# Kernel optimization log

Measured on AMD Instinct MI355X. Metric: run time of the kernel, lower is better.

Reference implementation:

```python
import jax, jax.numpy as jnp
import numpy as np


def setup_inputs() -> dict:
    key = jax.random.key(0)
    k1, k2 = jax.random.split(key)
    B, P, N, M = 8, 32, 1024, 1024
    normalized_receptive_fields = jax.random.normal(k1, (B, P, N, 3), dtype=jnp.float32)
    reconstructed_points = jax.random.normal(k2, (B, P, M, 3), dtype=jnp.float32)
    return {
        "normalized_receptive_fields": normalized_receptive_fields,
        "reconstructed_points": reconstructed_points,
    }


def reference(normalized_receptive_fields, reconstructed_points):
    B, P, M, _ = reconstructed_points.shape
    N = normalized_receptive_fields.shape[2]
    # Faithful to torch: permute(0,1,3,2) then reshape(-1, M, 3).
    x = jnp.transpose(reconstructed_points, (0, 1, 3, 2)).reshape(-1, M, 3)  # (BP, M, 3)
    y = normalized_receptive_fields.reshape(-1, N, 3)                        # (BP, N, 3)
    xx = jnp.sum(x * x, axis=-1)                 # (BP, M)
    yy = jnp.sum(y * y, axis=-1)                 # (BP, N)
    xy = jnp.einsum('bmc,bnc->bmn', x, y)        # (BP, M, N)
    dist = xx[:, :, None] + yy[:, None, :] - 2.0 * xy  # (BP, M, N)
    min_x_to_y = jnp.min(dist, axis=2)           # (BP, M)
    min_y_to_x = jnp.min(dist, axis=1)           # (BP, N)
    return jnp.mean(min_x_to_y) + jnp.mean(min_y_to_x)
```

## Files before the change

### kernel.cpp

```cpp
#include <hip/hip_runtime.h>
#include <hip/hip_bf16.h>


#define MM 1024
#define NN 1024
#define THREADS 1024
#define NWAVES 16
#define ROWS_PER_WAVE 64
#define RB 4
#define CPL 16
#define FINF 3.4e38f

template <int CTRL>
__device__ __forceinline__ float dpp_ror_min(float v) {
    int vi = __float_as_int(v);
    int t  = __builtin_amdgcn_update_dpp(vi, vi, CTRL, 0xf, 0xf, true);
    return fminf(v, __int_as_float(t));
}

__device__ __forceinline__ float wave_min64(float v, int lane_xor32_addr) {
    v = dpp_ror_min<0x121>(v);
    v = dpp_ror_min<0x122>(v);
    v = dpp_ror_min<0x124>(v);
    v = dpp_ror_min<0x128>(v);
    int s = __builtin_amdgcn_ds_swizzle(__float_as_int(v), 0x401F);
    v = fminf(v, __int_as_float(s));
    int p = __builtin_amdgcn_ds_bpermute(lane_xor32_addr, __float_as_int(v));
    return fminf(v, __int_as_float(p));
}

__global__ __launch_bounds__(THREADS, 4)
void chamfer_kernel(const float* __restrict__ nrf,
                    const float* __restrict__ rp,
                    float* __restrict__ out,
                    float inv_bpm, float inv_bpn) {
    const int bp   = blockIdx.x;
    const int tid  = threadIdx.x;
    const int lane = tid & 63;
    const int wave = tid >> 6;
    const int xaddr32 = ((lane ^ 32) << 2);

    __shared__ float  rpS[MM * 3];
    __shared__ float4 xS[MM];
    __shared__ float4 yS[NN];
    __shared__ float  colminS[NWAVES][NN];
    __shared__ float  rowsumS[NWAVES];
    __shared__ float  csumS[NWAVES];

    const float* rpB = rp  + (size_t)bp * MM * 3;
    const float* yB  = nrf + (size_t)bp * NN * 3;

    for (int i = tid; i < MM * 3; i += THREADS) rpS[i] = rpB[i];
    {
        float a = yB[tid * 3 + 0];
        float b = yB[tid * 3 + 1];
        float c = yB[tid * 3 + 2];
        yS[tid] = make_float4(a, b, c, a * a + b * b + c * c);
    }
    __syncthreads();

    {
        const int k = 3 * tid;
        float a = rpS[((k + 0) & (MM - 1)) * 3 + ((k + 0) >> 10)];
        float b = rpS[((k + 1) & (MM - 1)) * 3 + ((k + 1) >> 10)];
        float c = rpS[((k + 2) & (MM - 1)) * 3 + ((k + 2) >> 10)];
        xS[tid] = make_float4(-2.0f * a, -2.0f * b, -2.0f * c,
                              a * a + b * b + c * c);
    }
    __syncthreads();

    float colmin[CPL];
    #pragma unroll
    for (int i = 0; i < CPL; ++i) colmin[i] = FINF;

    float rowsum = 0.0f;
    const int m0 = wave * ROWS_PER_WAVE;
    for (int r0 = 0; r0 < ROWS_PER_WAVE; r0 += RB) {
        float4 x[RB];
        #pragma unroll
        for (int j = 0; j < RB; ++j) x[j] = xS[m0 + r0 + j];

        float rmin[RB];
        #pragma unroll
        for (int j = 0; j < RB; ++j) rmin[j] = FINF;

        #pragma unroll
        for (int i = 0; i < CPL; ++i) {
            const float4 yv = yS[i * 64 + lane];
            float e[RB];
            #pragma unroll
            for (int j = 0; j < RB; ++j) {
                e[j] = __builtin_fmaf(x[j].x, yv.x,
                        __builtin_fmaf(x[j].y, yv.y,
                         __builtin_fmaf(x[j].z, yv.z, yv.w)));
                rmin[j] = fminf(rmin[j], e[j]);
            }
            float d01 = fminf(e[0] + x[0].w, e[1] + x[1].w);
            float d23 = fminf(e[2] + x[2].w, e[3] + x[3].w);
            colmin[i] = fminf(fminf(colmin[i], d01), d23);
        }

        #pragma unroll
        for (int j = 0; j < RB; ++j) rmin[j] = wave_min64(rmin[j], xaddr32);
        #pragma unroll
        for (int j = 0; j < RB; ++j) rowsum += x[j].w + rmin[j];
    }

    #pragma unroll
    for (int i = 0; i < CPL; ++i) colminS[wave][i * 64 + lane] = colmin[i];
    if (lane == 0) rowsumS[wave] = rowsum;
    __syncthreads();

    {
        const int n = tid;
        float cm = colminS[0][n];
        #pragma unroll
        for (int w = 1; w < NWAVES; ++w) cm = fminf(cm, colminS[w][n]);
        float csum = cm;
        #pragma unroll
        for (int off = 32; off > 0; off >>= 1)
            csum += __shfl_xor(csum, off, 64);
        if (lane == 0) csumS[wave] = csum;
    }
    __syncthreads();

    if (tid == 0) {
        float rs = 0.0f, cs = 0.0f;
        #pragma unroll
        for (int w = 0; w < NWAVES; ++w) { rs += rowsumS[w]; cs += csumS[w]; }
        atomicAdd(out, rs * inv_bpm + cs * inv_bpn);
    }
}

extern "C" void kernel_launch(void* const* d_in, const int* in_sizes, int n_in,
                              void* d_out, int out_size, void* d_ws, size_t ws_size,
                              hipStream_t stream) {
    const float* nrf = (const float*)d_in[0];
    const float* rp  = (const float*)d_in[1];
    float* out = (float*)d_out;

    const int BP = in_sizes[1] / (MM * 3);
    const float inv_bpm = 1.0f / (float)(BP * MM);
    const float inv_bpn = 1.0f / (float)(BP * NN);

    (void)hipMemsetAsync(out, 0, sizeof(float), stream);
    chamfer_kernel<<<BP, THREADS, 0, stream>>>(nrf, rp, out, inv_bpm, inv_bpn);
}
```

Baseline: 97.19 us.

## Split each batch row range across four blocks with atomic-min column reduction

Each batch problem is now split across 4 blocks of 512 threads, each handling 256 rows, which raises the grid from 256 to 1024 blocks. Column minima are merged through order-preserving integer atomicMin, first in shared memory and then in a global workspace. The last block per batch, found via an atomic counter, sums the column minima. The row block size is raised to 8 for more reuse per y load. This adds memsets, global atomics and a fence-based last-block handshake in exchange for better occupancy and less shared-memory reduction work.

Result: slower. 348.1 us (+258.2%).

```diff
diff --git a/kernel.cpp b/kernel.cpp
--- a/kernel.cpp
+++ b/kernel.cpp
@@ -4,12 +4,23 @@
 
 #define MM 1024
 #define NN 1024
-#define THREADS 1024
-#define NWAVES 16
-#define ROWS_PER_WAVE 64
-#define RB 4
+#define THREADS 512
+#define NWAVES 8
+#define RBLK 4
+#define ROWS_PER_BLOCK 256
+#define ROWS_PER_WAVE 32
+#define RB 8
 #define CPL 16
 #define FINF 3.4e38f
+#define KEY_INIT 0x7F7F7F7F
+
+__device__ __forceinline__ int fkey(float f) {
+    int b = __float_as_int(f);
+    return (b >= 0) ? b : (b ^ 0x7FFFFFFF);
+}
+__device__ __forceinline__ float funkey(int k) {
+    return __int_as_float((k >= 0) ? k : (k ^ 0x7FFFFFFF));
+}
 
 template <int CTRL>
 __device__ __forceinline__ float dpp_ror_min(float v) {
@@ -17,53 +28,53 @@
     int t  = __builtin_amdgcn_update_dpp(vi, vi, CTRL, 0xf, 0xf, true);
     return fminf(v, __int_as_float(t));
 }
-
-__device__ __forceinline__ float wave_min64(float v, int lane_xor32_addr) {
+__device__ __forceinline__ float wave_min64(float v, int xaddr32) {
     v = dpp_ror_min<0x121>(v);
     v = dpp_ror_min<0x122>(v);
     v = dpp_ror_min<0x124>(v);
     v = dpp_ror_min<0x128>(v);
     int s = __builtin_amdgcn_ds_swizzle(__float_as_int(v), 0x401F);
     v = fminf(v, __int_as_float(s));
-    int p = __builtin_amdgcn_ds_bpermute(lane_xor32_addr, __float_as_int(v));
+    int p = __builtin_amdgcn_ds_bpermute(xaddr32, __float_as_int(v));
     return fminf(v, __int_as_float(p));
 }
 
-__global__ __launch_bounds__(THREADS, 4)
+__global__ __launch_bounds__(THREADS, 8)
 void chamfer_kernel(const float* __restrict__ nrf,
                     const float* __restrict__ rp,
                     float* __restrict__ out,
+                    int* __restrict__ wsKeys,
+                    int* __restrict__ wsCnt,
                     float inv_bpm, float inv_bpn) {
-    const int bp   = blockIdx.x;
+    const int bp   = blockIdx.x >> 2;
+    const int rb   = blockIdx.x & 3;
     const int tid  = threadIdx.x;
     const int lane = tid & 63;
     const int wave = tid >> 6;
     const int xaddr32 = ((lane ^ 32) << 2);
 
-    __shared__ float  rpS[MM * 3];
-    __shared__ float4 xS[MM];
     __shared__ float4 yS[NN];
-    __shared__ float  colminS[NWAVES][NN];
+    __shared__ float4 xS[ROWS_PER_BLOCK];
+    __shared__ int    colminI[NN];
     __shared__ float  rowsumS[NWAVES];
-    __shared__ float  csumS[NWAVES];
+    __shared__ int    lastS;
 
     const float* rpB = rp  + (size_t)bp * MM * 3;
     const float* yB  = nrf + (size_t)bp * NN * 3;
+    int* keysB = wsKeys + (size_t)bp * NN;
 
-    for (int i = tid; i < MM * 3; i += THREADS) rpS[i] = rpB[i];
-    {
-        float a = yB[tid * 3 + 0];
-        float b = yB[tid * 3 + 1];
-        float c = yB[tid * 3 + 2];
-        yS[tid] = make_float4(a, b, c, a * a + b * b + c * c);
+    #pragma unroll
+    for (int t = tid; t < NN; t += THREADS) {
+        float a = yB[t * 3 + 0], b = yB[t * 3 + 1], c = yB[t * 3 + 2];
+        yS[t] = make_float4(a, b, c, a * a + b * b + c * c);
+        colminI[t] = KEY_INIT;
     }
-    __syncthreads();
-
-    {
-        const int k = 3 * tid;
-        float a = rpS[((k + 0) & (MM - 1)) * 3 + ((k + 0) >> 10)];
-        float b = rpS[((k + 1) & (MM - 1)) * 3 + ((k + 1) >> 10)];
-        float c = rpS[((k + 2) & (MM - 1)) * 3 + ((k + 2) >> 10)];
+    if (tid < ROWS_PER_BLOCK) {
+        const int m = rb * ROWS_PER_BLOCK + tid;
+        const int k = 3 * m;
+        float a = rpB[((k + 0) & (MM - 1)) * 3 + ((k + 0) >> 10)];
+        float b = rpB[((k + 1) & (MM - 1)) * 3 + ((k + 1) >> 10)];
+        float c = rpB[((k + 2) & (MM - 1)) * 3 + ((k + 2) >> 10)];
         xS[tid] = make_float4(-2.0f * a, -2.0f * b, -2.0f * c,
                               a * a + b * b + c * c);
     }
@@ -95,9 +106,12 @@
                          __builtin_fmaf(x[j].z, yv.z, yv.w)));
                 rmin[j] = fminf(rmin[j], e[j]);
             }
-            float d01 = fminf(e[0] + x[0].w, e[1] + x[1].w);
-            float d23 = fminf(e[2] + x[2].w, e[3] + x[3].w);
-            colmin[i] = fminf(fminf(colmin[i], d01), d23);
+            float m01 = fminf(e[0] + x[0].w, e[1] + x[1].w);
+            float m23 = fminf(e[2] + x[2].w, e[3] + x[3].w);
+            float m45 = fminf(e[4] + x[4].w, e[5] + x[5].w);
+            float m67 = fminf(e[6] + x[6].w, e[7] + x[7].w);
+            colmin[i] = fminf(fminf(colmin[i], fminf(m01, m23)),
+                              fminf(m45, m67));
         }
 
         #pragma unroll
@@ -107,28 +121,43 @@
     }
 
     #pragma unroll
-    for (int i = 0; i < CPL; ++i) colminS[wave][i * 64 + lane] = colmin[i];
+    for (int i = 0; i < CPL; ++i)
+        atomicMin(&colminI[i * 64 + lane], fkey(colmin[i]));
     if (lane == 0) rowsumS[wave] = rowsum;
     __syncthreads();
 
-    {
-        const int n = tid;
-        float cm = colminS[0][n];
+    #pragma unroll
+    for (int t = tid; t < NN; t += THREADS)
+        atomicMin(&keysB[t], colminI[t]);
+    if (tid == 0) {
+        float rs = 0.0f;
         #pragma unroll
-        for (int w = 1; w < NWAVES; ++w) cm = fminf(cm, colminS[w][n]);
-        float csum = cm;
-        #pragma unroll
-        for (int off = 32; off > 0; off >>= 1)
-            csum += __shfl_xor(csum, off, 64);
-        if (lane == 0) csumS[wave] = csum;
+        for (int w = 0; w < NWAVES; ++w) rs += rowsumS[w];
+        atomicAdd(out, rs * inv_bpm);
+        __threadfence();
+        lastS = (atomicAdd(&wsCnt[bp], 1) == RBLK - 1);
     }
     __syncthreads();
 
-    if (tid == 0) {
-        float rs = 0.0f, cs = 0.0f;
+    if (lastS) {
+        __threadfence();
+        float cs = 0.0f;
         #pragma unroll
-        for (int w = 0; w < NWAVES; ++w) { rs += rowsumS[w]; cs += csumS[w]; }
-        atomicAdd(out, rs * inv_bpm + cs * inv_bpn);
+        for (int t = tid; t < NN; t += THREADS) {
+            int k = atomicMin(&keysB[t], 0x7FFFFFFF);
+            cs += funkey(k);
+        }
+        #pragma unroll
+        for (int off = 32; off > 0; off >>= 1)
+            cs += __shfl_xor(cs, off, 64);
+        if (lane == 0) rowsumS[wave] = cs;
+        __syncthreads();
+        if (tid == 0) {
+            float s = 0.0f;
+            #pragma unroll
+            for (int w = 0; w < NWAVES; ++w) s += rowsumS[w];
+            atomicAdd(out, s * inv_bpn);
+        }
     }
 }
 
@@ -143,6 +172,12 @@
     const float inv_bpm = 1.0f / (float)(BP * MM);
     const float inv_bpn = 1.0f / (float)(BP * NN);
 
+    int* wsKeys = (int*)d_ws;
+    int* wsCnt  = wsKeys + (size_t)BP * NN;
+
     (void)hipMemsetAsync(out, 0, sizeof(float), stream);
-    chamfer_kernel<<<BP, THREADS, 0, stream>>>(nrf, rp, out, inv_bpm, inv_bpn);
+    (void)hipMemsetAsync(wsKeys, 0x7F, (size_t)BP * NN * sizeof(int), stream);
+    (void)hipMemsetAsync(wsCnt, 0, (size_t)BP * sizeof(int), stream);
+    chamfer_kernel<<<BP * RBLK, THREADS, 0, stream>>>(
+        nrf, rp, out, wsKeys, wsCnt, inv_bpm, inv_bpn);
 }
```
